# Performance work log

Hardware: AMD Instinct MI355X
Metric: run time of the kernel (lower is better)

The kernel has to match this reference:

```python
import math
import jax, jax.numpy as jnp
import numpy as np

D_MODEL = 1024
N_HEAD = 16
HEAD_DIM = D_MODEL // N_HEAD  # 64
B = 8
L = 512
USE_GAUSSIAN = True
SCALE = 1.0  # scale=False in __init__


def rel_sin_pos_embed(seq_len, dim):
    # RelativeSinusoidalPositionalEmbedding: table row at index (pos+origin_shift)
    # holds [sin(pos*inv_freq), cos(pos*inv_freq)]; forward selects positions
    # arange(-L/2, round(L/2)) -> for even L this is -L/2 .. L/2-1.
    half = dim // 2
    inv_freq = jnp.exp(jnp.arange(half, dtype=jnp.float32) * (-math.log(10000.0) / (half - 1)))
    rel = jnp.arange(-(seq_len // 2), seq_len - seq_len // 2, dtype=jnp.float32)  # [L]
    ang = rel[:, None] * inv_freq[None, :]  # [L, half]
    return jnp.concatenate([jnp.sin(ang), jnp.cos(ang)], axis=-1)  # [L, dim]


def setup_inputs() -> dict:
    key = jax.random.key(0)
    ks = jax.random.split(key, 8)
    x = jax.random.normal(ks[0], (B, L, D_MODEL), dtype=jnp.float32)
    mask = jax.random.randint(ks[1], (B, L), 0, 2, dtype=jnp.int32)
    # guarantee at least one valid key per row so softmax never sees all -inf
    mask = mask.at[:, 0].set(1)
    qmask = jax.random.randint(ks[2], (B, L), 0, 2, dtype=jnp.int64)
    s = 0.02
    W_qkv = jax.random.normal(ks[3], (5 * D_MODEL, D_MODEL), dtype=jnp.float32) * s
    W_pos = jax.random.normal(ks[4], (3 * D_MODEL, HEAD_DIM), dtype=jnp.float32) * s
    W_fc = jax.random.normal(ks[5], (D_MODEL, D_MODEL), dtype=jnp.float32) * s
    b_fc = jnp.zeros((D_MODEL,), dtype=jnp.float32)
    # shift = abs(randn)+eps (positive), bias = -abs(randn); small scale keeps softmax sane
    shift = jnp.abs(jax.random.normal(ks[6], (1,), dtype=jnp.float32)) * 1e-4 + 1e-5
    bias = -jnp.abs(jax.random.normal(ks[7], (1,), dtype=jnp.float32))
    return {"x": x, "mask": mask, "qmask": qmask, "W_qkv": W_qkv, "W_pos": W_pos,
            "W_fc": W_fc, "b_fc": b_fc, "shift": shift, "bias": bias}


def reference(x, mask, qmask, W_qkv, W_pos, W_fc, b_fc, shift, bias):
    Bs, Ls, D = x.shape
    H, hd = N_HEAD, D // N_HEAD

    qkv = jnp.einsum('bld,ed->ble', x, W_qkv)  # [B, L, 5D]
    q, k, k1, k2, v = jnp.split(qkv, 5, axis=-1)

    def heads(t):  # [B, L, D] -> [B, H, L, hd]
        return t.reshape(Bs, Ls, H, hd).transpose(0, 2, 1, 3)

    q, k1, k2, v = heads(q), heads(k1), heads(k2), heads(v)

    pe = jax.lax.stop_gradient(rel_sin_pos_embed(Ls, hd))  # [L, hd], detached in torch
    y = jnp.einsum('ld,ed->le', pe, W_pos)  # [L, 3D]
    q_p, k1_p, k2_p = jnp.split(y, 3, axis=-1)
    q_p = q_p.reshape(Ls, H, hd).transpose(1, 0, 2)   # [H, L, hd]
    k1_p = k1_p.reshape(Ls, H, hd).transpose(1, 0, 2)  # [H, L, hd]
    k2_p = k2_p.reshape(Ls, H, hd).transpose(1, 0, 2)

    attn_self = jnp.einsum('bhid,bhjd->bhij', q, k1) + jnp.einsum('hid,hjd->hij', q_p, k1_p)[None]
    attn_others = jnp.einsum('bhid,bhjd->bhij', q, k2) + jnp.einsum('hid,hjd->hij', q_p, k2_p)[None]

    same = (qmask[:, :, None] == qmask[:, None, :])[:, None]  # [B, 1, L, L]
    attn = jnp.where(same, attn_self, 0.0) + jnp.where(same, 0.0, attn_others)
    attn = attn / SCALE
    attn = jnp.where(mask[:, None, None, :] == 0, -jnp.inf, attn)

    if USE_GAUSSIAN:
        idx = jnp.arange(Ls, dtype=jnp.float32)
        sq_dist = (idx[:, None] - idx[None, :]) ** 2  # [L, L]
        attn = attn + (-(shift[0] * sq_dist + bias[0]))[None, None]

    attn = jax.nn.softmax(attn, axis=-1)
    out = jnp.einsum('bhij,bhjd->bhid', attn, v)  # [B, H, L, hd]
    out = out.transpose(0, 2, 1, 3).reshape(Bs, Ls, D)
    return jnp.einsum('bld,ed->ble', out, W_fc) + b_fc
```

## Files before the change

kernel.cpp:

```cpp
#include <hip/hip_runtime.h>

#define DM 1024
#define HN 16
#define HD 64
#define BB 8
#define LL 512

typedef __bf16 bf16x8 __attribute__((ext_vector_type(8)));
typedef __bf16 bf16x4 __attribute__((ext_vector_type(4)));
typedef float  f32x4  __attribute__((ext_vector_type(4)));

__device__ __forceinline__ void cvt8(const float* __restrict__ in,
                                     __bf16* __restrict__ out, int i) {
    const float4* p = (const float4*)in + (size_t)i * 2;
    float4 a = p[0], b = p[1];
    bf16x8 v;
    v[0] = (__bf16)a.x; v[1] = (__bf16)a.y; v[2] = (__bf16)a.z; v[3] = (__bf16)a.w;
    v[4] = (__bf16)b.x; v[5] = (__bf16)b.y; v[6] = (__bf16)b.z; v[7] = (__bf16)b.w;
    ((bf16x8*)out)[i] = v;
}

__global__ __launch_bounds__(512) void prep_kernel(
    const int* __restrict__ qmask, const int* __restrict__ maskp,
    const float* __restrict__ x, const float* __restrict__ W_qkv,
    const float* __restrict__ W_pos, const float* __restrict__ W_fc,
    int* __restrict__ perm, int* __restrict__ pmask, float* __restrict__ posf,
    int* __restrict__ nzA, __bf16* __restrict__ PEb, __bf16* __restrict__ Wposb,
    __bf16* __restrict__ Wfcb, __bf16* __restrict__ Xb, __bf16* __restrict__ Wqkvb)
{
    const int blk = blockIdx.x, tid = threadIdx.x;
    if (blk < 8) {
        int b = blk, i = tid;
        int qm = qmask[b * LL + i];
        unsigned long long bz = __ballot(qm == 0);
        int wid = i >> 6, lane = i & 63;
        __shared__ int wz[8];
        int pzw = __popcll(bz & ((1ULL << lane) - 1ULL));
        if (lane == 0) wz[wid] = __popcll(bz);
        __syncthreads();
        int base = 0, nz = 0;
#pragma unroll
        for (int w2 = 0; w2 < 8; ++w2) { int c = wz[w2]; if (w2 < wid) base += c; nz += c; }
        int zbefore = base + pzw;
        int pos = (qm == 0) ? zbefore : (nz + (i - zbefore));
        perm[b * LL + pos] = i;
        pmask[b * LL + pos] = maskp[b * LL + i];
        posf[b * LL + pos] = (float)i;
        if (i == 0) nzA[b] = nz;
    } else if (blk < 72) {
        int idx = (blk - 8) * 512 + tid;
        int l = idx >> 6, d = idx & 63;
        float p = (float)(l - LL / 2);
        const float cexp = -9.210340371976184f / 31.0f;
        float val;
        if (d < 32) { float f = expf((float)d * cexp);        val = sinf(p * f); }
        else        { float f = expf((float)(d - 32) * cexp); val = cosf(p * f); }
        PEb[idx] = (__bf16)val;
    } else if (blk < 120) {
        cvt8(W_pos, Wposb, (blk - 72) * 512 + tid);
    } else if (blk < 376) {
        cvt8(W_fc, Wfcb, (blk - 120) * 512 + tid);
    } else if (blk < 1400) {
        cvt8(x, Xb, (blk - 376) * 512 + tid);
    } else if (blk < 1656) {
        cvt8(W_qkv, Wqkvb, (blk - 1400) * 512 + tid);
    } else {
        cvt8(W_qkv + 2097152, Wqkvb + 1048576, (blk - 1656) * 512 + tid);
    }
}

template<int MODE>
__global__ __launch_bounds__(256, 4) void gemm_mfma(
    const __bf16* __restrict__ A, const __bf16* __restrict__ Bm,
    __bf16* __restrict__ Qc, __bf16* __restrict__ K1c,
    __bf16* __restrict__ K2c, __bf16* __restrict__ Vn,
    float* __restrict__ outF, const float* __restrict__ bias, int K)
{
    __shared__ __bf16 smem[128 * 136];
    __bf16* As = smem;
    __bf16* Bs = smem + 8192;
    __bf16* Cs = smem;
    const int tid = threadIdx.x;
    const int lane = tid & 63;
    const int w = tid >> 6;
    const int wm = w >> 1, wn = w & 1;
    const int n0 = blockIdx.x * 128;
    const int m0 = blockIdx.y * 128;
    const int fr = lane & 15;
    const int fq = lane >> 4;

    const int srow = tid >> 3;
    const int scol = (tid & 7) ^ (srow & 7);
    const __bf16* Ag = A + (size_t)(m0 + srow) * K + scol * 8;
    const __bf16* Bg = Bm + (size_t)(n0 + srow) * K + scol * 8;
    char* AsB = (char*)As + (size_t)w * 1024;
    char* BsB = (char*)Bs + (size_t)w * 1024;

    f32x4 acc[4][4] = {};

    for (int k0 = 0; k0 < K; k0 += 64) {
#pragma unroll
        for (int r = 0; r < 4; ++r) {
            __builtin_amdgcn_global_load_lds(Ag + k0 + (size_t)(r * 32) * K, AsB + r * 4096, 16, 0, 0);
            __builtin_amdgcn_global_load_lds(Bg + k0 + (size_t)(r * 32) * K, BsB + r * 4096, 16, 0, 0);
        }
        __syncthreads();

#pragma unroll
        for (int kk = 0; kk < 2; ++kk) {
            const int so = ((kk * 4 + fq) ^ (fr & 7)) * 8;
            bf16x8 af[4], bfr[4];
#pragma unroll
            for (int i = 0; i < 4; ++i)
                af[i] = *(const bf16x8*)(As + (size_t)(wm * 64 + i * 16 + fr) * 64 + so);
#pragma unroll
            for (int j = 0; j < 4; ++j)
                bfr[j] = *(const bf16x8*)(Bs + (size_t)(wn * 64 + j * 16 + fr) * 64 + so);
#pragma unroll
            for (int i = 0; i < 4; ++i)
#pragma unroll
                for (int j = 0; j < 4; ++j)
                    acc[i][j] = __builtin_amdgcn_mfma_f32_16x16x32_bf16(bfr[j], af[i], acc[i][j], 0, 0, 0);
        }
        __syncthreads();
    }

    if constexpr (MODE == 0 || MODE == 2) {
#pragma unroll
        for (int i = 0; i < 4; ++i) {
            int mloc = wm * 64 + i * 16 + fr;
#pragma unroll
            for (int j = 0; j < 4; ++j) {
                int nloc = wn * 64 + j * 16 + fq * 4;
                bf16x4 v;
#pragma unroll
                for (int r = 0; r < 4; ++r) v[r] = (__bf16)acc[i][j][r];
                *(bf16x4*)(Cs + (size_t)mloc * 136 + nloc) = v;
            }
        }
        __syncthreads();
        if constexpr (MODE == 0) {
            const int c = n0 >> 10;
            __bf16* T = (c == 0) ? Qc : (c == 1) ? K1c : (c == 2) ? K2c : Vn;
            const int b = m0 >> 9, l0 = m0 & 511, h0 = (n0 >> 6) & 15;
#pragma unroll
            for (int rnd = 0; rnd < 8; ++rnd) {
                int Ci = rnd * 256 + tid;
                int m = Ci >> 4, nch = Ci & 15;
                bf16x8 v = *(const bf16x8*)(Cs + (size_t)m * 136 + nch * 8);
                int hl = nch >> 3, d = (nch & 7) * 8;
                size_t bh2 = (size_t)(b * HN + h0 + hl);
                if (c < 3) *(bf16x8*)(T + (bh2 * LL + l0 + m) * 128 + d) = v;
                else       *(bf16x8*)(T + (bh2 * LL + l0 + m) * 64  + d) = v;
            }
        } else {
            const int c = n0 >> 10;
            __bf16* T = (c == 0) ? Qc : (c == 1) ? K1c : K2c;
#pragma unroll
            for (int rnd = 0; rnd < 8; ++rnd) {
                int Ci = rnd * 256 + tid;
                int m = Ci >> 4, nch = Ci & 15;
                bf16x8 v = *(const bf16x8*)(Cs + (size_t)m * 136 + nch * 8);
                int eg = n0 + nch * 8;
                int h = (eg >> 6) & 15, d = eg & 63;
                size_t off = ((size_t)h * LL + (m0 + m)) * 128 + 64 + d;
#pragma unroll
                for (int b = 0; b < 8; ++b)
                    *(bf16x8*)(T + (size_t)b * (HN * LL * 128) + off) = v;
            }
        }
    } else {
#pragma unroll
        for (int i = 0; i < 4; ++i) {
            int m = m0 + wm * 64 + i * 16 + fr;
#pragma unroll
            for (int j = 0; j < 4; ++j) {
                int nn = n0 + wn * 64 + j * 16 + fq * 4;
                float4 bv = *(const float4*)(bias + nn);
                *(float4*)(outF + (size_t)m * DM + nn) =
                    make_float4(acc[i][j][0] + bv.x, acc[i][j][1] + bv.y,
                                acc[i][j][2] + bv.z, acc[i][j][3] + bv.w);
            }
        }
    }
}

__global__ __launch_bounds__(256) void vtrans_kernel(const __bf16* __restrict__ Vn,
                                                     const int* __restrict__ perm,
                                                     __bf16* __restrict__ Vt) {
    __shared__ __bf16 Ts[64][72];
    int bh = blockIdx.x >> 3, lt = blockIdx.x & 7;
    int b = bh >> 4;
    int r = threadIdx.x >> 2, s = threadIdx.x & 3;
    int orow = perm[b * LL + lt * 64 + r];
    const __bf16* src = Vn + ((size_t)bh * LL + orow) * 64;
    *(bf16x8*)&Ts[r][s * 16]     = *(const bf16x8*)(src + s * 16);
    *(bf16x8*)&Ts[r][s * 16 + 8] = *(const bf16x8*)(src + s * 16 + 8);
    __syncthreads();
    __bf16* dst = Vt + ((size_t)bh * 64 + r) * LL + lt * 64 + s * 16;
    bf16x8 a, bvv;
#pragma unroll
    for (int e = 0; e < 8; ++e) { a[e] = Ts[s * 16 + e][r]; bvv[e] = Ts[s * 16 + 8 + e][r]; }
    *(bf16x8*)dst = a;
    *(bf16x8*)(dst + 8) = bvv;
}

__global__ __launch_bounds__(512, 2) void attn_kernel(
    const __bf16* __restrict__ Qc, const __bf16* __restrict__ K1c,
    const __bf16* __restrict__ K2c, const __bf16* __restrict__ Vt,
    const int* __restrict__ pmask, const int* __restrict__ perm,
    const float* __restrict__ posf, const int* __restrict__ nzA,
    const float* __restrict__ shiftp, const float* __restrict__ biasp,
    __bf16* __restrict__ AO)
{
    __shared__ __bf16 Ke0[64 * 136];
    __shared__ __bf16 Ke1[64 * 136];
    __shared__ __bf16 Vts[64 * 88];
    __shared__ __bf16 Sb[8 * 16 * 72];
    __shared__ __align__(16) float posL[64];

    const int tid = threadIdx.x;
    const int lane = tid & 63;
    const int wid = tid >> 6;
    const int fr = lane & 15;
    const int fq = lane >> 4;

    const int bid = (blockIdx.x & 7) * 64 + (blockIdx.x >> 3);
    const int qt = bid & 3;
    const int h  = (bid >> 2) & 15;
    const int b  = bid >> 6;
    const size_t bh = (size_t)(b * HN + h);
    const int nz = nzA[b];
    const int q0blk = qt * 128;
    const int s = q0blk + wid * 16 + fr;
    const int pi = perm[b * LL + s];
    const bool need0 = (q0blk < nz);
    const bool need1 = (q0blk + 127 >= nz);
    const int w0 = q0blk + wid * 16;
    const bool wneed0 = (w0 < nz);
    const bool wneed1 = (w0 + 15 >= nz);
    const int qmI = (s >= nz) ? 1 : 0;

    const float sft = shiftp[0];

    bf16x8 qf[4];
    {
        const __bf16* qrow = Qc + (bh * LL + pi) * 128;
#pragma unroll
        for (int kf = 0; kf < 4; ++kf)
            qf[kf] = *(const bf16x8*)(qrow + kf * 32 + fq * 8);
    }

    float mrun = -1e30f, lrun = 0.f;
    f32x4 ot[4] = {};
    const float qposf = (float)pi;

    const __bf16* K1g0 = K1c + bh * LL * 128;
    const __bf16* K2g0 = K2c + bh * LL * 128;
    const __bf16* Vtg0 = Vt + bh * 64 * LL;
    __bf16* Sw = Sb + wid * 16 * 72;

    const int krr = tid >> 4;
    const int ku  = tid & 15;
    const int vrr = tid >> 3;
    const int vu  = tid & 7;

    bf16x8 rk0[2], rk1[2], rv;
    int pm; float ppos;

#define LOAD_TILE(tt)                                                              \
    {                                                                              \
        int j0_ = (tt) * 64;                                                       \
        _Pragma("unroll")                                                          \
        for (int p = 0; p < 2; ++p) {                                              \
            int sr = j0_ + p * 32 + krr;                                           \
            int orow = perm[b * LL + sr];                                          \
            int qmj = (sr >= nz) ? 1 : 0;                                          \
            const __bf16* s1 = (qmj ? K2g0 : K1g0) + (size_t)orow * 128 + ku * 8;  \
            const __bf16* s2 = (qmj ? K1g0 : K2g0) + (size_t)orow * 128 + ku * 8;  \
            if (need0) rk0[p] = *(const bf16x8*)s1;                                \
            if (need1) rk1[p] = *(const bf16x8*)s2;                                \
        }                                                                          \
        rv = *(const bf16x8*)(Vtg0 + (size_t)vrr * LL + j0_ + vu * 8);             \
        pm = pmask[b * LL + j0_ + lane];                                           \
        ppos = posf[b * LL + j0_ + lane];                                          \
    }

    LOAD_TILE(0);

    for (int t = 0; t < 8; ++t) {
        __syncthreads();
        {
#pragma unroll
            for (int p = 0; p < 2; ++p) {
                int rr = p * 32 + krr;
                if (need0) *(bf16x8*)(Ke0 + rr * 136 + ku * 8) = rk0[p];
                if (need1) *(bf16x8*)(Ke1 + rr * 136 + ku * 8) = rk1[p];
            }
            *(bf16x8*)(Vts + vrr * 88 + vu * 8) = rv;
            if (wid == 0) posL[lane] = ppos;
        }
        unsigned long long kbits = __ballot(pm != 0);
        if (t < 7) LOAD_TILE(t + 1);
        __syncthreads();

        f32x4 acc[4];
        if (wneed0 != wneed1) {
            const __bf16* Ks = wneed0 ? Ke0 : Ke1;
            __builtin_amdgcn_s_setprio(1);
#pragma unroll
            for (int kb = 0; kb < 4; ++kb) {
                bf16x8 af[4];
#pragma unroll
                for (int kf = 0; kf < 4; ++kf)
                    af[kf] = *(const bf16x8*)(Ks + (kb * 16 + fr) * 136 + kf * 32 + fq * 8);
                f32x4 a = {};
#pragma unroll
                for (int kf = 0; kf < 4; ++kf)
                    a = __builtin_amdgcn_mfma_f32_16x16x32_bf16(af[kf], qf[kf], a, 0, 0, 0);
                acc[kb] = a;
            }
            __builtin_amdgcn_s_setprio(0);
        } else {
            __builtin_amdgcn_s_setprio(1);
#pragma unroll
            for (int kb = 0; kb < 4; ++kb) {
                bf16x8 a0f[4], a1f[4];
#pragma unroll
                for (int kf = 0; kf < 4; ++kf) {
                    a0f[kf] = *(const bf16x8*)(Ke0 + (kb * 16 + fr) * 136 + kf * 32 + fq * 8);
                    a1f[kf] = *(const bf16x8*)(Ke1 + (kb * 16 + fr) * 136 + kf * 32 + fq * 8);
                }
                f32x4 t0 = {}, t1 = {};
#pragma unroll
                for (int kf = 0; kf < 4; ++kf) {
                    t0 = __builtin_amdgcn_mfma_f32_16x16x32_bf16(a0f[kf], qf[kf], t0, 0, 0, 0);
                    t1 = __builtin_amdgcn_mfma_f32_16x16x32_bf16(a1f[kf], qf[kf], t1, 0, 0, 0);
                }
#pragma unroll
                for (int r = 0; r < 4; ++r) acc[kb][r] = qmI ? t1[r] : t0[r];
            }
            __builtin_amdgcn_s_setprio(0);
        }

#pragma unroll
        for (int kb = 0; kb < 4; ++kb) {
            f32x4 pj = *(const f32x4*)(posL + kb * 16 + fq * 4);
#pragma unroll
            for (int r = 0; r < 4; ++r) {
                float di = qposf - pj[r];
                acc[kb][r] -= sft * di * di;
            }
        }

        float lmax = acc[0][0];
#pragma unroll
        for (int kb = 0; kb < 4; ++kb)
#pragma unroll
            for (int r = 0; r < 4; ++r) lmax = fmaxf(lmax, acc[kb][r]);
        if (!__all(lmax <= mrun + 8.f)) {
            float mn = fmaxf(mrun, lmax);
            mn = fmaxf(mn, __shfl_xor(mn, 16));
            mn = fmaxf(mn, __shfl_xor(mn, 32));
            float sc = __expf(mrun - mn);
            mrun = mn;
            lrun *= sc;
#pragma unroll
            for (int fd = 0; fd < 4; ++fd)
#pragma unroll
                for (int r = 0; r < 4; ++r) ot[fd][r] *= sc;
        }
        float sum = 0.f;
#pragma unroll
        for (int kb = 0; kb < 4; ++kb)
#pragma unroll
            for (int r = 0; r < 4; ++r) {
                int ko = kb * 16 + fq * 4 + r;
                float p = ((int)(kbits >> ko) & 1) ? __expf(acc[kb][r] - mrun) : 0.f;
                acc[kb][r] = p;
                sum += p;
            }
        sum += __shfl_xor(sum, 16);
        sum += __shfl_xor(sum, 32);
        lrun += sum;

#pragma unroll
        for (int kb = 0; kb < 4; ++kb) {
            bf16x4 pk;
#pragma unroll
            for (int r = 0; r < 4; ++r) pk[r] = (__bf16)acc[kb][r];
            *(bf16x4*)(Sw + fr * 72 + kb * 16 + fq * 4) = pk;
        }
        bf16x8 pf0 = *(const bf16x8*)(Sw + fr * 72 + fq * 8);
        bf16x8 pf1 = *(const bf16x8*)(Sw + fr * 72 + 32 + fq * 8);
        __builtin_amdgcn_s_setprio(1);
#pragma unroll
        for (int fd = 0; fd < 4; ++fd) {
            bf16x8 v0 = *(const bf16x8*)(Vts + (fd * 16 + fr) * 88 + fq * 8);
            bf16x8 v1 = *(const bf16x8*)(Vts + (fd * 16 + fr) * 88 + 32 + fq * 8);
            ot[fd] = __builtin_amdgcn_mfma_f32_16x16x32_bf16(v0, pf0, ot[fd], 0, 0, 0);
            ot[fd] = __builtin_amdgcn_mfma_f32_16x16x32_bf16(v1, pf1, ot[fd], 0, 0, 0);
        }
        __builtin_amdgcn_s_setprio(0);
    }
#undef LOAD_TILE

    {
        const float inv = 1.0f / lrun;
#pragma unroll
        for (int fd = 0; fd < 4; ++fd) {
            bf16x4 o;
#pragma unroll
            for (int r = 0; r < 4; ++r) o[r] = (__bf16)(ot[fd][r] * inv);
            *(bf16x4*)(Sw + fr * 72 + fd * 16 + fq * 4) = o;
        }
    }
    __syncthreads();
    {
        int r = tid >> 2, c = tid & 3;
        int pir = perm[b * LL + q0blk + r];
        const __bf16* src = Sb + (r >> 4) * (16 * 72) + (r & 15) * 72;
        __bf16* dst = AO + ((size_t)(b * LL + pir)) * DM + h * 64;
        *(bf16x8*)(dst + c * 8)      = *(const bf16x8*)(src + c * 8);
        *(bf16x8*)(dst + 32 + c * 8) = *(const bf16x8*)(src + 32 + c * 8);
    }
}

extern "C" void kernel_launch(void* const* d_in, const int* in_sizes, int n_in,
                              void* d_out, int out_size, void* d_ws, size_t ws_size,
                              hipStream_t stream) {
    const float* x     = (const float*)d_in[0];
    const int*   mask  = (const int*)d_in[1];
    const int*   qmask = (const int*)d_in[2];
    const float* W_qkv = (const float*)d_in[3];
    const float* W_pos = (const float*)d_in[4];
    const float* W_fc  = (const float*)d_in[5];
    const float* b_fc  = (const float*)d_in[6];
    const float* shift = (const float*)d_in[7];
    const float* bias  = (const float*)d_in[8];
    float* out = (float*)d_out;

    __bf16* Qcb  = (__bf16*)d_ws;
    __bf16* K1cb = Qcb  + 8388608;
    __bf16* K2cb = K1cb + 8388608;
    __bf16* Vnb  = K2cb + 8388608;
    __bf16* Vtb  = Vnb  + 4194304;
    __bf16* Xb   = Vtb  + 4194304;
    __bf16* Wqkvb = Xb  + 4194304;
    __bf16* AOb   = Xb;
    __bf16* PEb   = Wqkvb + 4194304;
    __bf16* Wposb = PEb + 32768;
    __bf16* Wfcb  = Wposb + 196608;
    int* permA = (int*)(Wfcb + 1048576);
    int* nzA   = permA + 4096;
    int* pmaskA = nzA + 8;
    float* posfA = (float*)(pmaskA + 4096);

    prep_kernel<<<2424, 512, 0, stream>>>(qmask, mask, x, W_qkv, W_pos, W_fc,
                                          permA, pmaskA, posfA, nzA,
                                          PEb, Wposb, Wfcb, Xb, Wqkvb);
    gemm_mfma<0><<<dim3(32, 32), 256, 0, stream>>>(Xb, Wqkvb, Qcb, K1cb, K2cb, Vnb,
                                                   nullptr, nullptr, 1024);
    vtrans_kernel<<<1024, 256, 0, stream>>>(Vnb, permA, Vtb);
    gemm_mfma<2><<<dim3(24, 4), 256, 0, stream>>>(PEb, Wposb, Qcb, K1cb, K2cb, nullptr,
                                                  nullptr, nullptr, 64);
    attn_kernel<<<512, 512, 0, stream>>>(Qcb, K1cb, K2cb, Vtb, pmaskA, permA,
                                         posfA, nzA, shift, bias, AOb);
    gemm_mfma<1><<<dim3(8, 32), 256, 0, stream>>>(AOb, Wfcb, nullptr, nullptr, nullptr,
                                                  nullptr, out, b_fc, 1024);
}
```

Before: 132.0 us.

## Fuse QKV and positional GEMMs into one launch; schedule attention blocks by workload

Merges the QKV projection GEMM and the small positional-embedding GEMM into a single grid of 1120 blocks, with block-index branching, which removes one kernel launch and the tail of the small GEMM. The prep kernel now builds a schedule table so that, for each (batch, head), the query tile that straddles the qmask boundary (and so evaluates both score branches) is dispatched first, followed by the remaining tiles. The goal is better load balance across CUs. The bias parameter is dropped from the attention kernel signature, which presumably was unused. The costs are a data-dependent schedule read at attention start and divergent index math in the fused GEMM.

```diff
diff --git a/kernel.cpp b/kernel.cpp
--- a/kernel.cpp
+++ b/kernel.cpp
@@ -25,7 +25,8 @@
     const float* __restrict__ x, const float* __restrict__ W_qkv,
     const float* __restrict__ W_pos, const float* __restrict__ W_fc,
     int* __restrict__ perm, int* __restrict__ pmask, float* __restrict__ posf,
-    int* __restrict__ nzA, __bf16* __restrict__ PEb, __bf16* __restrict__ Wposb,
+    int* __restrict__ nzA, int* __restrict__ sched,
+    __bf16* __restrict__ PEb, __bf16* __restrict__ Wposb,
     __bf16* __restrict__ Wfcb, __bf16* __restrict__ Xb, __bf16* __restrict__ Wqkvb)
 {
     const int blk = blockIdx.x, tid = threadIdx.x;
@@ -47,6 +48,18 @@
         pmask[b * LL + pos] = maskp[b * LL + i];
         posf[b * LL + pos] = (float)i;
         if (i == 0) nzA[b] = nz;
+        if (i < 16) {
+            int bh2 = b * 16 + i;
+            int g = i & 7;
+            int idx = b * 2 + (i >> 3);
+            int qtm = nz >> 7; if (qtm > 3) qtm = 3;
+            sched[idx * 8 + g] = (bh2 << 2) | qtm;
+#pragma unroll
+            for (int j = 0; j < 3; ++j) {
+                int qtj = j + (j >= qtm ? 1 : 0);
+                sched[(16 + idx * 3 + j) * 8 + g] = (bh2 << 2) | qtj;
+            }
+        }
     } else if (blk < 72) {
         int idx = (blk - 8) * 512 + tid;
         int l = idx >> 6, d = idx & 63;
@@ -69,12 +82,11 @@
     }
 }
 
-template<int MODE>
-__global__ __launch_bounds__(256, 4) void gemm_mfma(
-    const __bf16* __restrict__ A, const __bf16* __restrict__ Bm,
+__global__ __launch_bounds__(256, 4) void gemm_fused(
+    const __bf16* __restrict__ Xb, const __bf16* __restrict__ Wqkvb,
+    const __bf16* __restrict__ PEb, const __bf16* __restrict__ Wposb,
     __bf16* __restrict__ Qc, __bf16* __restrict__ K1c,
-    __bf16* __restrict__ K2c, __bf16* __restrict__ Vn,
-    float* __restrict__ outF, const float* __restrict__ bias, int K)
+    __bf16* __restrict__ K2c, __bf16* __restrict__ Vn)
 {
     __shared__ __bf16 smem[128 * 136];
     __bf16* As = smem;
@@ -84,8 +96,15 @@
     const int lane = tid & 63;
     const int w = tid >> 6;
     const int wm = w >> 1, wn = w & 1;
-    const int n0 = blockIdx.x * 128;
-    const int m0 = blockIdx.y * 128;
+
+    const bool isPos = (blockIdx.x >= 1024);
+    const int bi = isPos ? (blockIdx.x - 1024) : blockIdx.x;
+    const int n0 = isPos ? (bi % 24) * 128 : (bi & 31) * 128;
+    const int m0 = isPos ? (bi / 24) * 128 : (bi >> 5) * 128;
+    const int K  = isPos ? 64 : 1024;
+    const __bf16* A  = isPos ? PEb : Xb;
+    const __bf16* Bm = isPos ? Wposb : Wqkvb;
+
     const int fr = lane & 15;
     const int fq = lane >> 4;
 
@@ -125,62 +144,114 @@
         __syncthreads();
     }
 
-    if constexpr (MODE == 0 || MODE == 2) {
-#pragma unroll
-        for (int i = 0; i < 4; ++i) {
-            int mloc = wm * 64 + i * 16 + fr;
-#pragma unroll
-            for (int j = 0; j < 4; ++j) {
-                int nloc = wn * 64 + j * 16 + fq * 4;
-                bf16x4 v;
-#pragma unroll
-                for (int r = 0; r < 4; ++r) v[r] = (__bf16)acc[i][j][r];
-                *(bf16x4*)(Cs + (size_t)mloc * 136 + nloc) = v;
-            }
-        }
-        __syncthreads();
-        if constexpr (MODE == 0) {
-            const int c = n0 >> 10;
-            __bf16* T = (c == 0) ? Qc : (c == 1) ? K1c : (c == 2) ? K2c : Vn;
-            const int b = m0 >> 9, l0 = m0 & 511, h0 = (n0 >> 6) & 15;
-#pragma unroll
-            for (int rnd = 0; rnd < 8; ++rnd) {
-                int Ci = rnd * 256 + tid;
-                int m = Ci >> 4, nch = Ci & 15;
-                bf16x8 v = *(const bf16x8*)(Cs + (size_t)m * 136 + nch * 8);
-                int hl = nch >> 3, d = (nch & 7) * 8;
-                size_t bh2 = (size_t)(b * HN + h0 + hl);
-                if (c < 3) *(bf16x8*)(T + (bh2 * LL + l0 + m) * 128 + d) = v;
-                else       *(bf16x8*)(T + (bh2 * LL + l0 + m) * 64  + d) = v;
-            }
-        } else {
-            const int c = n0 >> 10;
-            __bf16* T = (c == 0) ? Qc : (c == 1) ? K1c : K2c;
-#pragma unroll
-            for (int rnd = 0; rnd < 8; ++rnd) {
-                int Ci = rnd * 256 + tid;
-                int m = Ci >> 4, nch = Ci & 15;
-                bf16x8 v = *(const bf16x8*)(Cs + (size_t)m * 136 + nch * 8);
-                int eg = n0 + nch * 8;
-                int h = (eg >> 6) & 15, d = eg & 63;
-                size_t off = ((size_t)h * LL + (m0 + m)) * 128 + 64 + d;
-#pragma unroll
-                for (int b = 0; b < 8; ++b)
-                    *(bf16x8*)(T + (size_t)b * (HN * LL * 128) + off) = v;
-            }
+#pragma unroll
+    for (int i = 0; i < 4; ++i) {
+        int mloc = wm * 64 + i * 16 + fr;
+#pragma unroll
+        for (int j = 0; j < 4; ++j) {
+            int nloc = wn * 64 + j * 16 + fq * 4;
+            bf16x4 v;
+#pragma unroll
+            for (int r = 0; r < 4; ++r) v[r] = (__bf16)acc[i][j][r];
+            *(bf16x4*)(Cs + (size_t)mloc * 136 + nloc) = v;
+        }
+    }
+    __syncthreads();
+    if (!isPos) {
+        const int c = n0 >> 10;
+        __bf16* T = (c == 0) ? Qc : (c == 1) ? K1c : (c == 2) ? K2c : Vn;
+        const int b = m0 >> 9, l0 = m0 & 511, h0 = (n0 >> 6) & 15;
+#pragma unroll
+        for (int rnd = 0; rnd < 8; ++rnd) {
+            int Ci = rnd * 256 + tid;
+            int m = Ci >> 4, nch = Ci & 15;
+            bf16x8 v = *(const bf16x8*)(Cs + (size_t)m * 136 + nch * 8);
+            int hl = nch >> 3, d = (nch & 7) * 8;
+            size_t bh2 = (size_t)(b * HN + h0 + hl);
+            if (c < 3) *(bf16x8*)(T + (bh2 * LL + l0 + m) * 128 + d) = v;
+            else       *(bf16x8*)(T + (bh2 * LL + l0 + m) * 64  + d) = v;
         }
     } else {
-#pragma unroll
-        for (int i = 0; i < 4; ++i) {
-            int m = m0 + wm * 64 + i * 16 + fr;
-#pragma unroll
-            for (int j = 0; j < 4; ++j) {
-                int nn = n0 + wn * 64 + j * 16 + fq * 4;
-                float4 bv = *(const float4*)(bias + nn);
-                *(float4*)(outF + (size_t)m * DM + nn) =
-                    make_float4(acc[i][j][0] + bv.x, acc[i][j][1] + bv.y,
-                                acc[i][j][2] + bv.z, acc[i][j][3] + bv.w);
-            }
+        const int c = n0 >> 10;
+        __bf16* T = (c == 0) ? Qc : (c == 1) ? K1c : K2c;
+#pragma unroll
+        for (int rnd = 0; rnd < 8; ++rnd) {
+            int Ci = rnd * 256 + tid;
+            int m = Ci >> 4, nch = Ci & 15;
+            bf16x8 v = *(const bf16x8*)(Cs + (size_t)m * 136 + nch * 8);
+            int eg = n0 + nch * 8;
+            int h = (eg >> 6) & 15, d = eg & 63;
+            size_t off = ((size_t)h * LL + (m0 + m)) * 128 + 64 + d;
+#pragma unroll
+            for (int b = 0; b < 8; ++b)
+                *(bf16x8*)(T + (size_t)b * (HN * LL * 128) + off) = v;
+        }
+    }
+}
+
+__global__ __launch_bounds__(256, 4) void gemm_out(
+    const __bf16* __restrict__ A, const __bf16* __restrict__ Bm,
+    float* __restrict__ outF, const float* __restrict__ bias)
+{
+    __shared__ __bf16 smem[128 * 136];
+    __bf16* As = smem;
+    __bf16* Bs = smem + 8192;
+    const int tid = threadIdx.x;
+    const int lane = tid & 63;
+    const int w = tid >> 6;
+    const int wm = w >> 1, wn = w & 1;
+    const int n0 = blockIdx.x * 128;
+    const int m0 = blockIdx.y * 128;
+    const int fr = lane & 15;
+    const int fq = lane >> 4;
+    const int K = 1024;
+
+    const int srow = tid >> 3;
+    const int scol = (tid & 7) ^ (srow & 7);
+    const __bf16* Ag = A + (size_t)(m0 + srow) * K + scol * 8;
+    const __bf16* Bg = Bm + (size_t)(n0 + srow) * K + scol * 8;
+    char* AsB = (char*)As + (size_t)w * 1024;
+    char* BsB = (char*)Bs + (size_t)w * 1024;
+
+    f32x4 acc[4][4] = {};
+
+    for (int k0 = 0; k0 < K; k0 += 64) {
+#pragma unroll
+        for (int r = 0; r < 4; ++r) {
+            __builtin_amdgcn_global_load_lds(Ag + k0 + (size_t)(r * 32) * K, AsB + r * 4096, 16, 0, 0);
+            __builtin_amdgcn_global_load_lds(Bg + k0 + (size_t)(r * 32) * K, BsB + r * 4096, 16, 0, 0);
+        }
+        __syncthreads();
+
+#pragma unroll
+        for (int kk = 0; kk < 2; ++kk) {
+            const int so = ((kk * 4 + fq) ^ (fr & 7)) * 8;
+            bf16x8 af[4], bfr[4];
+#pragma unroll
+            for (int i = 0; i < 4; ++i)
+                af[i] = *(const bf16x8*)(As + (size_t)(wm * 64 + i * 16 + fr) * 64 + so);
+#pragma unroll
+            for (int j = 0; j < 4; ++j)
+                bfr[j] = *(const bf16x8*)(Bs + (size_t)(wn * 64 + j * 16 + fr) * 64 + so);
+#pragma unroll
+            for (int i = 0; i < 4; ++i)
+#pragma unroll
+                for (int j = 0; j < 4; ++j)
+                    acc[i][j] = __builtin_amdgcn_mfma_f32_16x16x32_bf16(bfr[j], af[i], acc[i][j], 0, 0, 0);
+        }
+        __syncthreads();
+    }
+
+#pragma unroll
+    for (int i = 0; i < 4; ++i) {
+        int m = m0 + wm * 64 + i * 16 + fr;
+#pragma unroll
+        for (int j = 0; j < 4; ++j) {
+            int nn = n0 + wn * 64 + j * 16 + fq * 4;
+            float4 bv = *(const float4*)(bias + nn);
+            *(float4*)(outF + (size_t)m * DM + nn) =
+                make_float4(acc[i][j][0] + bv.x, acc[i][j][1] + bv.y,
+                            acc[i][j][2] + bv.z, acc[i][j][3] + bv.w);
         }
     }
 }
@@ -210,8 +281,8 @@
     const __bf16* __restrict__ K2c, const __bf16* __restrict__ Vt,
     const int* __restrict__ pmask, const int* __restrict__ perm,
     const float* __restrict__ posf, const int* __restrict__ nzA,
-    const float* __restrict__ shiftp, const float* __restrict__ biasp,
-    __bf16* __restrict__ AO)
+    const int* __restrict__ sched,
+    const float* __restrict__ shiftp, __bf16* __restrict__ AO)
 {
     __shared__ __bf16 Ke0[64 * 136];
     __shared__ __bf16 Ke1[64 * 136];
@@ -225,10 +296,10 @@
     const int fr = lane & 15;
     const int fq = lane >> 4;
 
-    const int bid = (blockIdx.x & 7) * 64 + (blockIdx.x >> 3);
-    const int qt = bid & 3;
-    const int h  = (bid >> 2) & 15;
-    const int b  = bid >> 6;
+    const int e = sched[blockIdx.x];
+    const int qt = e & 3;
+    const int h  = (e >> 2) & 15;
+    const int b  = e >> 6;
     const size_t bh = (size_t)(b * HN + h);
     const int nz = nzA[b];
     const int q0blk = qt * 128;
@@ -455,17 +526,15 @@
     int* nzA   = permA + 4096;
     int* pmaskA = nzA + 8;
     float* posfA = (float*)(pmaskA + 4096);
+    int* schedA = (int*)(posfA + 4096);
 
     prep_kernel<<<2424, 512, 0, stream>>>(qmask, mask, x, W_qkv, W_pos, W_fc,
-                                          permA, pmaskA, posfA, nzA,
+                                          permA, pmaskA, posfA, nzA, schedA,
                                           PEb, Wposb, Wfcb, Xb, Wqkvb);
-    gemm_mfma<0><<<dim3(32, 32), 256, 0, stream>>>(Xb, Wqkvb, Qcb, K1cb, K2cb, Vnb,
-                                                   nullptr, nullptr, 1024);
+    gemm_fused<<<1120, 256, 0, stream>>>(Xb, Wqkvb, PEb, Wposb,
+                                         Qcb, K1cb, K2cb, Vnb);
     vtrans_kernel<<<1024, 256, 0, stream>>>(Vnb, permA, Vtb);
-    gemm_mfma<2><<<dim3(24, 4), 256, 0, stream>>>(PEb, Wposb, Qcb, K1cb, K2cb, nullptr,
-                                                  nullptr, nullptr, 64);
     attn_kernel<<<512, 512, 0, stream>>>(Qcb, K1cb, K2cb, Vtb, pmaskA, permA,
-                                         posfA, nzA, shift, bias, AOb);
-    gemm_mfma<1><<<dim3(8, 32), 256, 0, stream>>>(AOb, Wfcb, nullptr, nullptr, nullptr,
-                                                  nullptr, out, b_fc, 1024);
-}
+                                         posfA, nzA, schedA, shift, AOb);
+    gemm_out<<<dim3(8, 32), 256, 0, stream>>>(AOb, Wfcb, out, b_fc);
+}
```

Measured after the change: 127.3 us. 3.6% less time.
